# Kernel tuning notes

Measured on AMD Instinct MI355X. Metric: run time of the kernel, lower is better.

Reference implementation:

```python
import jax, jax.numpy as jnp
import numpy as np

WS = (8, 8, 8)          # window_size (d, h, w) -- all equal
N_TOK = WS[0] * WS[1] * WS[2]   # 512
DIM = 192
HEADS = 6
HEAD_DIM = DIM // HEADS  # 32
B_ = 64                  # num_windows * batch (batch = 1)


def _build_rel_coords_table():
    # matches torch: meshgrid of arange(-(w-1), w) per axis, normalized, *8, signed log2
    r = np.arange(-(WS[0] - 1), WS[0], dtype=np.float32)
    tab = np.stack(np.meshgrid(r, r, r, indexing='ij'), axis=-1)[None]  # (1,15,15,15,3)
    tab = tab / (WS[0] - 1)
    tab = tab * 8.0
    tab = np.sign(tab) * np.log2(np.abs(tab) + 1.0) / np.log2(8.0)
    return tab.astype(np.float32)


def _build_rel_pos_index():
    c = np.arange(WS[0])
    coords = np.stack(np.meshgrid(c, c, c, indexing='ij'))          # (3, 8, 8, 8)
    flat = coords.reshape(3, -1)                                     # (3, N)
    rel = flat[:, :, None] - flat[:, None, :]                        # (3, N, N)
    rel = rel.transpose(1, 2, 0).copy()                              # (N, N, 3)
    rel += WS[0] - 1
    rel[:, :, 0] *= (2 * WS[1] - 1) * (2 * WS[2] - 1)
    rel[:, :, 1] *= 2 * WS[2] - 1
    return rel.sum(-1).astype(np.int32)                              # (N, N)


def setup_inputs() -> dict:
    key = jax.random.key(0)
    ks = jax.random.split(key, 8)
    x = jax.random.normal(ks[0], (B_, N_TOK, DIM), dtype=jnp.float32)
    # 0 / -inf style additive mask (use large negative finite for stability)
    m = jax.random.uniform(ks[1], (B_, N_TOK, N_TOK))
    mask = jnp.where(m < 0.1, jnp.float32(-1e4), jnp.float32(0.0))
    w_qkv = jax.random.normal(ks[2], (3 * DIM, DIM), dtype=jnp.float32) * (DIM ** -0.5)
    q_bias = jnp.zeros((DIM,), jnp.float32)
    v_bias = jnp.zeros((DIM,), jnp.float32)
    cpb_w1 = jax.random.normal(ks[3], (512, 3), dtype=jnp.float32) * 0.3
    cpb_b1 = jnp.zeros((512,), jnp.float32)
    cpb_w2 = jax.random.normal(ks[4], (HEADS, 512), dtype=jnp.float32) * 0.05
    rel_coords_table = jnp.asarray(_build_rel_coords_table())
    rel_pos_index = jnp.asarray(_build_rel_pos_index())
    return {"x": x, "mask": mask, "w_qkv": w_qkv, "q_bias": q_bias,
            "v_bias": v_bias, "cpb_w1": cpb_w1, "cpb_b1": cpb_b1,
            "cpb_w2": cpb_w2, "rel_coords_table": rel_coords_table,
            "rel_pos_index": rel_pos_index}


def reference(x, mask, w_qkv, q_bias, v_bias, cpb_w1, cpb_b1, cpb_w2,
              rel_coords_table, rel_pos_index):
    Bw, N, C = x.shape
    H, D = HEADS, HEAD_DIM
    # qkv projection with bias = cat(q_bias, zeros, v_bias)
    qkv_bias = jnp.concatenate([q_bias, jnp.zeros_like(v_bias), v_bias])
    qkv = x @ w_qkv.T + qkv_bias                       # (Bw, N, 3C)
    qkv = qkv.reshape(Bw, N, 3, H, D).transpose(2, 0, 3, 1, 4)
    q, k, v = qkv[0], qkv[1], qkv[2]                   # (Bw, H, N, D)
    # continuous position bias MLP: 3 -> 512 -> H
    tab = rel_coords_table.reshape(-1, 3)              # (3375, 3)
    tab = jax.nn.relu(tab @ cpb_w1.T + cpb_b1) @ cpb_w2.T  # (3375, H)
    bias = tab[rel_pos_index.reshape(-1)].reshape(N, N, H)
    bias = 16.0 * jax.nn.sigmoid(bias.transpose(2, 0, 1))  # (H, N, N)
    # SDPA with additive mask (standard 1/sqrt(D) scaling, as in forward_flash)
    scale = jnp.float32(1.0 / np.sqrt(D))
    scores = jnp.einsum('bhnd,bhmd->bhnm', q, k) * scale
    scores = scores + mask[:, None, :, :] + bias[None]
    attn = jax.nn.softmax(scores, axis=-1)
    out = jnp.einsum('bhnm,bhmd->bhnd', attn, v)       # (Bw, H, N, D)
    return out
```

## Files before the change

kernel.cpp:

```cpp
#include <hip/hip_runtime.h>
#include <hip/hip_bf16.h>


typedef __bf16 bf16x8 __attribute__((ext_vector_type(8)));
typedef __bf16 bf16x4v __attribute__((ext_vector_type(4)));
typedef float  f32x4  __attribute__((ext_vector_type(4)));
typedef _Float16 f16x4 __attribute__((ext_vector_type(4)));
typedef _Float16 f16x8 __attribute__((ext_vector_type(8)));
typedef unsigned uint2v __attribute__((ext_vector_type(2)));
typedef int int4v __attribute__((ext_vector_type(4)));
typedef unsigned long long u64;

#define LOG2E 1.4426950408889634f

__device__ __forceinline__ bf16x8 cvt2_bf16x8(f32x4 a, f32x4 b) {
  bf16x8 r;
  r[0] = (__bf16)a[0]; r[1] = (__bf16)a[1]; r[2] = (__bf16)a[2]; r[3] = (__bf16)a[3];
  r[4] = (__bf16)b[0]; r[5] = (__bf16)b[1]; r[6] = (__bf16)b[2]; r[7] = (__bf16)b[3];
  return r;
}

__device__ __forceinline__ unsigned pack2bf(float a, float b) {
  unsigned short ua = __builtin_bit_cast(unsigned short, (__bf16)a);
  unsigned short ub = __builtin_bit_cast(unsigned short, (__bf16)b);
  return (unsigned)ua | ((unsigned)ub << 16);
}

__device__ __forceinline__ bf16x8 frag_from_words(unsigned w0, unsigned w1,
                                                  unsigned w2, unsigned w3) {
  union { unsigned u[4]; bf16x8 v; } f;
  f.u[0] = w0; f.u[1] = w1; f.u[2] = w2; f.u[3] = w3;
  return f.v;
}

#define PREP_WCONV 108
#define PREP_CPB   3375
#define PREP_WC    (PREP_WCONV + PREP_CPB)
#define PREP_MB    2048
#define PREP_GRID  (PREP_WC + PREP_MB)

__global__ __launch_bounds__(256) void prep_kernel(
    const float* __restrict__ w, __bf16* __restrict__ wbf,
    const float* __restrict__ table, const float* __restrict__ w1,
    const float* __restrict__ b1, const float* __restrict__ w2,
    float* __restrict__ tab6,
    const float* __restrict__ m, u64* __restrict__ bits)
{
  __shared__ float red[4][6];
  int blk = blockIdx.x;
  if (blk < PREP_WCONV) {
    int t = blk * 256 + threadIdx.x;
    f32x4 v = *(const f32x4*)(w + (size_t)t * 4);
    bf16x4v o;
    o[0] = (__bf16)v[0]; o[1] = (__bf16)v[1]; o[2] = (__bf16)v[2]; o[3] = (__bf16)v[3];
    *(bf16x4v*)(wbf + (size_t)t * 4) = o;
  } else if (blk < PREP_WC) {
    int p = blk - PREP_WCONV;
    float c0 = table[p * 3 + 0], c1 = table[p * 3 + 1], c2 = table[p * 3 + 2];
    float acc[6] = {0.f, 0.f, 0.f, 0.f, 0.f, 0.f};
#pragma unroll
    for (int jj = 0; jj < 2; ++jj) {
      int j = threadIdx.x + jj * 256;
      float hv = w1[j * 3 + 0] * c0 + w1[j * 3 + 1] * c1 + w1[j * 3 + 2] * c2 + b1[j];
      hv = fmaxf(hv, 0.0f);
#pragma unroll
      for (int t = 0; t < 6; ++t) acc[t] += w2[t * 512 + j] * hv;
    }
#pragma unroll
    for (int t = 0; t < 6; ++t) {
      acc[t] += __shfl_xor(acc[t], 1);
      acc[t] += __shfl_xor(acc[t], 2);
      acc[t] += __shfl_xor(acc[t], 4);
      acc[t] += __shfl_xor(acc[t], 8);
      acc[t] += __shfl_xor(acc[t], 16);
      acc[t] += __shfl_xor(acc[t], 32);
    }
    int wave = threadIdx.x >> 6;
    if ((threadIdx.x & 63) == 0)
#pragma unroll
      for (int t = 0; t < 6; ++t) red[wave][t] = acc[t];
    __syncthreads();
    if (threadIdx.x < 6) {
      int t = threadIdx.x;
      float s = red[0][t] + red[1][t] + red[2][t] + red[3][t];
      float sig = 16.0f / (1.0f + expf(-s));
      tab6[p * 8 + t] = sig * LOG2E;
    }
  } else {
    int li8 = threadIdx.x & 7;
    for (size_t t = (size_t)(blk - PREP_WC) * 256 + threadIdx.x;
         t < 2097152ull; t += (size_t)PREP_MB * 256) {
      const float* mp = m + t * 8;
      f32x4 v0 = *(const f32x4*)mp;
      f32x4 v1 = *(const f32x4*)(mp + 4);
      unsigned byte =
          (v0[0] == 0.f ? 1u : 0u)  | (v0[1] == 0.f ? 2u : 0u) |
          (v0[2] == 0.f ? 4u : 0u)  | (v0[3] == 0.f ? 8u : 0u) |
          (v1[0] == 0.f ? 16u : 0u) | (v1[1] == 0.f ? 32u : 0u) |
          (v1[2] == 0.f ? 64u : 0u) | (v1[3] == 0.f ? 128u : 0u);
      u64 part = (u64)byte << (8 * li8);
      part |= __shfl_xor(part, 1);
      part |= __shfl_xor(part, 2);
      part |= __shfl_xor(part, 4);
      if (li8 == 0) {
        int w_ = (int)(t >> 3);
        int b = w_ >> 12, i = (w_ >> 3) & 511, jw = w_ & 7;
        bits[(((size_t)b * 8 + jw) << 9) + i] = part;
      }
    }
  }
}

#define MID_QKV  1024
#define MID_BIAS 342
#define MID_GRID (MID_QKV + MID_BIAS)

__global__ __launch_bounds__(192) void mid_kernel(
    const float* __restrict__ x,
    const __bf16* __restrict__ wbf,
    const float* __restrict__ qb,
    const float* __restrict__ vb,
    __bf16* __restrict__ Qo,
    __bf16* __restrict__ Ko,
    __bf16* __restrict__ Vt,
    const int* __restrict__ relidx,
    const float* __restrict__ tab6,
    _Float16* __restrict__ biasH)
{
  __shared__ __bf16 tile[2][32][72];
  if (blockIdx.x >= MID_QKV) {
    for (int q4 = (blockIdx.x - MID_QKV) * 192 + threadIdx.x; q4 < 65536;
         q4 += MID_BIAS * 192) {
      int ij = q4 * 4;
      int i = ij >> 9, p = ij & 511;
      int jblk = p >> 6, g = (p >> 4) & 3, kf = (p >> 2) & 3;
      int j = (jblk << 6) + kf * 16 + g * 4;
      int4v idx4 = *(const int4v*)(relidx + (i << 9) + j);
      float val[6][4];
#pragma unroll
      for (int u = 0; u < 4; ++u) {
        f32x4 lo = *(const f32x4*)(tab6 + (size_t)idx4[u] * 8);
        f32x4 hi = *(const f32x4*)(tab6 + (size_t)idx4[u] * 8 + 4);
        val[0][u] = lo[0]; val[1][u] = lo[1]; val[2][u] = lo[2];
        val[3][u] = lo[3]; val[4][u] = hi[0]; val[5][u] = hi[1];
      }
#pragma unroll
      for (int t6 = 0; t6 < 6; ++t6) {
        f16x4 o = {(_Float16)val[t6][0], (_Float16)val[t6][1],
                   (_Float16)val[t6][2], (_Float16)val[t6][3]};
        *(f16x4*)(biasH + (size_t)t6 * 262144 + ij) = o;
      }
    }
    return;
  }
  const float CQ = 0.17677669529663687f * LOG2E;
  int lane = threadIdx.x & 63, wave = threadIdx.x >> 6;
  int g = lane >> 4, li = lane & 15;
  int rowbase = blockIdx.x * 32;
  int b = rowbase >> 9, nbase = rowbase & 511;

  bf16x8 a[2][6];
#pragma unroll
  for (int mm = 0; mm < 2; ++mm)
#pragma unroll
    for (int k = 0; k < 6; ++k) {
      const float* xp = x + (size_t)(rowbase + mm * 16 + li) * 192 + k * 32 + 8 * g;
      f32x4 x0 = *(const f32x4*)xp;
      f32x4 x1 = *(const f32x4*)(xp + 4);
      a[mm][k] = cvt2_bf16x8(x0, x1);
    }

  for (int ncl = 0; ncl < 3; ++ncl) {
    int nc = wave * 3 + ncl;
    f32x4 acc[2][4];
#pragma unroll
    for (int n = 0; n < 4; ++n) {
      int r = nc * 64 + n * 16 + li;
      float bb = 0.0f;
      if (r < 192) bb = qb[r];
      else if (r >= 384) bb = vb[r - 384];
      f32x4 v = {bb, bb, bb, bb};
      acc[0][n] = v; acc[1][n] = v;
    }
#pragma unroll
    for (int k = 0; k < 6; ++k) {
#pragma unroll
      for (int n = 0; n < 4; ++n) {
        bf16x8 bf = *(const bf16x8*)(wbf + (size_t)(nc * 64 + n * 16 + li) * 192 + k * 32 + 8 * g);
        acc[0][n] = __builtin_amdgcn_mfma_f32_16x16x32_bf16(a[0][k], bf, acc[0][n], 0, 0, 0);
        acc[1][n] = __builtin_amdgcn_mfma_f32_16x16x32_bf16(a[1][k], bf, acc[1][n], 0, 0, 0);
      }
    }
    if (wave < 2) {
      float scale = (wave == 0) ? CQ : 1.0f;
#pragma unroll
      for (int n = 0; n < 4; ++n)
#pragma unroll
        for (int mm = 0; mm < 2; ++mm)
#pragma unroll
          for (int t = 0; t < 4; ++t)
            tile[wave][mm * 16 + 4 * g + t][n * 16 + li] = (__bf16)(acc[mm][n][t] * scale);
      int tok = lane & 31, hh = lane >> 5;
      int h = (nc * 2 + hh) % 6;
      __bf16* base = (wave == 0) ? Qo : Ko;
      __bf16* dst = base + ((size_t)(b * 6 + h) * 512 + nbase + tok) * 32;
#pragma unroll
      for (int kq = 0; kq < 4; ++kq)
        *(bf16x8*)(dst + kq * 8) = *(const bf16x8*)&tile[wave][tok][hh * 32 + kq * 8];
    } else {
#pragma unroll
      for (int n = 0; n < 4; ++n) {
        int rr = nc * 64 + n * 16 + li - 384, h = rr >> 5, d = rr & 31;
#pragma unroll
        for (int mm = 0; mm < 2; ++mm) {
          int nn = nbase + mm * 16 + 4 * g;
          bf16x4v pk;
#pragma unroll
          for (int t = 0; t < 4; ++t) pk[t] = (__bf16)acc[mm][n][t];
          *(bf16x4v*)(Vt + ((size_t)(b * 6 + h) * 32 + d) * 512 + nn) = pk;
        }
      }
    }
  }
}

__global__ __launch_bounds__(256, 3) void attn_kernel(
    const u64* __restrict__ bits,
    const _Float16* __restrict__ biasH,
    const __bf16* __restrict__ Qw,
    const __bf16* __restrict__ Kw,
    const __bf16* __restrict__ Vt,
    float* __restrict__ out)
{
  int hw = blockIdx.x;
  int wgid = (hw & 7) * 96 + (hw >> 3);
  int qt = wgid & 1, h = (wgid >> 1) % 6, b = wgid / 12;
  int lane = threadIdx.x & 63, wave = threadIdx.x >> 6;
  int g = lane >> 4, li = lane & 15;
  int qbase = qt * 256 + wave * 64;
  int bh = b * 6 + h;
  int gsh = 4 * g;

  const __bf16* Qb = Qw + (size_t)bh * 16384;
  const __bf16* Kb = Kw + (size_t)bh * 16384;
  const __bf16* Vb = Vt + (size_t)bh * 16384;
  const _Float16* biasb = biasH + (size_t)h * 262144 + g * 16;
  const u64* bitsb = bits + (size_t)b * 4096;

  bf16x8 qfrag[4];
#pragma unroll
  for (int qf = 0; qf < 4; ++qf)
    qfrag[qf] = *(const bf16x8*)(Qb + (qbase + qf * 16 + li) * 32 + 8 * g);

  f32x4 oacc[4][2] = {};
  float l_part[4] = {0.f, 0.f, 0.f, 0.f};

  for (int kb = 0; kb < 8; ++kb) {
    int j64 = kb * 64;
    u64 mb[4];
#pragma unroll
    for (int qf = 0; qf < 4; ++qf)
      mb[qf] = bitsb[(kb << 9) + qbase + qf * 16 + li] >> gsh;
    bf16x8 kfr[4];
#pragma unroll
    for (int kf = 0; kf < 4; ++kf)
      kfr[kf] = *(const bf16x8*)(Kb + (j64 + kf * 16 + li) * 32 + 8 * g);
    bf16x8 vfr[2][2];
#pragma unroll
    for (int df = 0; df < 2; ++df)
#pragma unroll
      for (int c = 0; c < 2; ++c)
        vfr[df][c] = *(const bf16x8*)(Vb + (df * 16 + li) * 512 + j64 + c * 32 + 8 * g);
    f16x8 hv8[4][2];
#pragma unroll
    for (int qf = 0; qf < 4; ++qf) {
      const _Float16* bp = biasb + (size_t)(qbase + qf * 16 + li) * 512 + j64;
      hv8[qf][0] = *(const f16x8*)(bp);
      hv8[qf][1] = *(const f16x8*)(bp + 8);
    }

#pragma unroll
    for (int c = 0; c < 2; ++c) {
      unsigned lo[4][2], hi[4][2];
#pragma unroll
      for (int kfl = 0; kfl < 2; ++kfl) {
        int kf = c * 2 + kfl;
        const int hsel = kf >> 1, hoff = (kf & 1) * 4;
#pragma unroll
        for (int qf = 0; qf < 4; ++qf) {
          f16x8 hb = hv8[qf][hsel];
          f32x4 ci = {(float)hb[hoff], (float)hb[hoff + 1],
                      (float)hb[hoff + 2], (float)hb[hoff + 3]};
          f32x4 s = __builtin_amdgcn_mfma_f32_16x16x32_bf16(kfr[kf], qfrag[qf], ci, 0, 0, 0);
          unsigned nib = (unsigned)(mb[qf] >> (kf * 16)) & 15u;
          float p0 = (nib & 1u) ? __builtin_amdgcn_exp2f(s[0]) : 0.0f;
          float p1 = (nib & 2u) ? __builtin_amdgcn_exp2f(s[1]) : 0.0f;
          float p2 = (nib & 4u) ? __builtin_amdgcn_exp2f(s[2]) : 0.0f;
          float p3 = (nib & 8u) ? __builtin_amdgcn_exp2f(s[3]) : 0.0f;
          l_part[qf] += (p0 + p1) + (p2 + p3);
          lo[qf][kfl] = pack2bf(p0, p1);
          hi[qf][kfl] = pack2bf(p2, p3);
        }
      }
#pragma unroll
      for (int qf = 0; qf < 4; ++qf) {
        uint2v sl = __builtin_amdgcn_permlane32_swap(lo[qf][0], lo[qf][1], 0, 0);
        uint2v wl = __builtin_amdgcn_permlane16_swap(sl.x, sl.y, 0, 0);
        uint2v sh = __builtin_amdgcn_permlane32_swap(hi[qf][0], hi[qf][1], 0, 0);
        uint2v wh = __builtin_amdgcn_permlane16_swap(sh.x, sh.y, 0, 0);
        bf16x8 pf = frag_from_words(wl.x, wh.x, wl.y, wh.y);
#pragma unroll
        for (int df = 0; df < 2; ++df)
          oacc[qf][df] = __builtin_amdgcn_mfma_f32_16x16x32_bf16(vfr[df][c], pf, oacc[qf][df], 0, 0, 0);
      }
    }
  }

#pragma unroll
  for (int qf = 0; qf < 4; ++qf) {
    float l = l_part[qf];
    l += __shfl_xor(l, 16);
    l += __shfl_xor(l, 32);
    float linv = 1.0f / l;
#pragma unroll
    for (int df = 0; df < 2; ++df) {
      float* op = out + ((size_t)bh * 512 + qbase + qf * 16 + li) * 32 + df * 16 + 4 * g;
      f32x4 r = oacc[qf][df] * linv;
      *(f32x4*)op = r;
    }
  }
}

extern "C" void kernel_launch(void* const* d_in, const int* in_sizes, int n_in,
                              void* d_out, int out_size, void* d_ws, size_t ws_size,
                              hipStream_t stream) {
  const float* x    = (const float*)d_in[0];
  const float* mask = (const float*)d_in[1];
  const float* wqkv = (const float*)d_in[2];
  const float* qb   = (const float*)d_in[3];
  const float* vb   = (const float*)d_in[4];
  const float* w1   = (const float*)d_in[5];
  const float* b1   = (const float*)d_in[6];
  const float* w2   = (const float*)d_in[7];
  const float* tbl  = (const float*)d_in[8];
  const int*   ridx = (const int*)d_in[9];
  float* out = (float*)d_out;

  char* ws = (char*)d_ws;
  float*    tab6  = (float*)(ws);
  _Float16* biasH = (_Float16*)(ws + 131072);
  u64*      bits  = (u64*)(ws + 131072 + 3145728);
  __bf16*   wbf   = (__bf16*)(ws + 131072 + 3145728 + 2097152);
  __bf16*   Q     = (__bf16*)(ws + 131072 + 3145728 + 2097152 + 262144);
  __bf16*   K     = Q + (size_t)64 * 6 * 512 * 32;
  __bf16*   Vt    = K + (size_t)64 * 6 * 512 * 32;

  prep_kernel<<<PREP_GRID, 256, 0, stream>>>(wqkv, wbf, tbl, w1, b1, w2, tab6,
                                             mask, bits);
  mid_kernel<<<MID_GRID, 192, 0, stream>>>(x, wbf, qb, vb, Q, K, Vt,
                                           ridx, tab6, biasH);
  attn_kernel<<<768, 256, 0, stream>>>(bits, biasH, Q, K, Vt, out);
}
```

Baseline: 118.1 us.

## Split key loop across two wave groups and reduce partials via LDS

Doubles the attention block to 512 threads, with two wave groups each processing half of the key blocks for the same query rows. The second group writes its partial output accumulators and row sums to shared memory, and the first group adds them in before normalizing and storing. This raises the number of waves in flight and shortens each wave's serial loop, to hide memory and MFMA latency better. It costs an LDS buffer, a block barrier, and tighter register limits from the new launch bounds, which could cause spills.

Result: slower. 306.4 us (+159.3%).

```diff
diff --git a/kernel.cpp b/kernel.cpp
--- a/kernel.cpp
+++ b/kernel.cpp
@@ -224,7 +224,7 @@
   }
 }
 
-__global__ __launch_bounds__(256, 3) void attn_kernel(
+__global__ __launch_bounds__(512, 6) void attn_kernel(
     const u64* __restrict__ bits,
     const _Float16* __restrict__ biasH,
     const __bf16* __restrict__ Qw,
@@ -232,12 +232,15 @@
     const __bf16* __restrict__ Vt,
     float* __restrict__ out)
 {
+  __shared__ float oshare[4][64][37];
+
   int hw = blockIdx.x;
   int wgid = (hw & 7) * 96 + (hw >> 3);
   int qt = wgid & 1, h = (wgid >> 1) % 6, b = wgid / 12;
   int lane = threadIdx.x & 63, wave = threadIdx.x >> 6;
+  int wq = wave & 3, ws_ = wave >> 2;
   int g = lane >> 4, li = lane & 15;
-  int qbase = qt * 256 + wave * 64;
+  int qbase = qt * 256 + wq * 64;
   int bh = b * 6 + h;
   int gsh = 4 * g;
 
@@ -255,7 +258,8 @@
   f32x4 oacc[4][2] = {};
   float l_part[4] = {0.f, 0.f, 0.f, 0.f};
 
-  for (int kb = 0; kb < 8; ++kb) {
+  int kb0 = ws_ * 4;
+  for (int kb = kb0; kb < kb0 + 4; ++kb) {
     int j64 = kb * 64;
     u64 mb[4];
 #pragma unroll
@@ -316,17 +320,40 @@
     }
   }
 
-#pragma unroll
-  for (int qf = 0; qf < 4; ++qf) {
-    float l = l_part[qf];
-    l += __shfl_xor(l, 16);
-    l += __shfl_xor(l, 32);
-    float linv = 1.0f / l;
-#pragma unroll
-    for (int df = 0; df < 2; ++df) {
-      float* op = out + ((size_t)bh * 512 + qbase + qf * 16 + li) * 32 + df * 16 + 4 * g;
-      f32x4 r = oacc[qf][df] * linv;
-      *(f32x4*)op = r;
+  if (ws_ == 1) {
+    float* dst = &oshare[wq][lane][0];
+#pragma unroll
+    for (int qf = 0; qf < 4; ++qf)
+#pragma unroll
+      for (int df = 0; df < 2; ++df)
+#pragma unroll
+        for (int t = 0; t < 4; ++t) dst[qf * 8 + df * 4 + t] = oacc[qf][df][t];
+#pragma unroll
+    for (int qf = 0; qf < 4; ++qf) dst[32 + qf] = l_part[qf];
+  }
+  __syncthreads();
+  if (ws_ == 0) {
+    const float* src = &oshare[wq][lane][0];
+#pragma unroll
+    for (int qf = 0; qf < 4; ++qf) {
+#pragma unroll
+      for (int df = 0; df < 2; ++df)
+#pragma unroll
+        for (int t = 0; t < 4; ++t) oacc[qf][df][t] += src[qf * 8 + df * 4 + t];
+      l_part[qf] += src[32 + qf];
+    }
+#pragma unroll
+    for (int qf = 0; qf < 4; ++qf) {
+      float l = l_part[qf];
+      l += __shfl_xor(l, 16);
+      l += __shfl_xor(l, 32);
+      float linv = 1.0f / l;
+#pragma unroll
+      for (int df = 0; df < 2; ++df) {
+        float* op = out + ((size_t)bh * 512 + qbase + qf * 16 + li) * 32 + df * 16 + 4 * g;
+        f32x4 r = oacc[qf][df] * linv;
+        *(f32x4*)op = r;
+      }
     }
   }
 }
@@ -359,5 +386,5 @@
                                              mask, bits);
   mid_kernel<<<MID_GRID, 192, 0, stream>>>(x, wbf, qb, vb, Q, K, Vt,
                                            ridx, tab6, biasH);
-  attn_kernel<<<768, 256, 0, stream>>>(bits, biasH, Q, K, Vt, out);
-}
+  attn_kernel<<<768, 512, 0, stream>>>(bits, biasH, Q, K, Vt, out);
+}
```
